# Kernel optimization log

Hardware: AMD Instinct MI355X
Metric: run time of the kernel (lower is better)

## Reference

```python
import jax, jax.numpy as jnp
import numpy as np

B, SQ, SK = 2, 2048, 2048
E = 256   # embed_dim (also per-head key dim in this MHA)
S = 256   # srcdim (also per-head value dim)
NH = 8    # num_heads
HID = 2 * S  # FFN hidden = in_dim * 2


def setup_inputs() -> dict:
    key = jax.random.key(0)
    ks = jax.random.split(key, 12)
    def w(k, shape, s=0.02):
        return jax.random.normal(k, shape, dtype=jnp.float32) * s
    return {
        "Q": jax.random.normal(ks[0], (B, SQ, E), dtype=jnp.float32),
        "H": jax.random.normal(ks[1], (B, SK, E), dtype=jnp.float32),
        "A": jax.random.normal(ks[2], (B, SK, S), dtype=jnp.float32),
        # MHA params (torch Linear convention: y = x @ W.T + b)
        "wq": w(ks[3], (NH * E, E)), "bq": jnp.zeros((NH * E,), jnp.float32),
        "wk": w(ks[4], (NH * E, E)), "bk": jnp.zeros((NH * E,), jnp.float32),
        "wv": w(ks[5], (NH * S, S)), "bv": jnp.zeros((NH * S,), jnp.float32),
        "wo": w(ks[6], (S, NH * S)), "bo": jnp.zeros((S,), jnp.float32),
        # Attension scale (Parameter(torch.ones(1)))
        "attn_scale": jnp.ones((), jnp.float32),
        # shared LayerNormA params
        "ln_g": jnp.ones((S,), jnp.float32), "ln_b": jnp.zeros((S,), jnp.float32),
        # FFN params
        "w1": w(ks[7], (HID, S)), "b1": jnp.zeros((HID,), jnp.float32),
        "w2": w(ks[8], (S, HID)), "b2": jnp.zeros((S,), jnp.float32),
    }


def _layernorm(x, g, b, eps=1e-5):
    m = x.mean(-1, keepdims=True)
    v = ((x - m) ** 2).mean(-1, keepdims=True)
    return (x - m) / jnp.sqrt(v + eps) * g + b


def reference(Q, H, A, wq, bq, wk, bk, wv, bv, wo, bo,
              attn_scale, ln_g, ln_b, w1, b1, w2, b2):
    b_, sq, _ = Q.shape
    sk = H.shape[1]
    # ---- MHA branch (A_m) ----
    q = (Q @ wq.T + bq).reshape(b_, sq, NH, E).transpose(0, 2, 1, 3)  # [b,h,sq,E]
    k = (H @ wk.T + bk).reshape(b_, sk, NH, E).transpose(0, 2, 1, 3)  # [b,h,sk,E]
    v = (A @ wv.T + bv).reshape(b_, sk, NH, S).transpose(0, 2, 1, 3)  # [b,h,sk,S]
    scores = jnp.einsum('bhqe,bhke->bhqk', q, k) / jnp.sqrt(jnp.float32(E))
    probs = jax.nn.softmax(scores, axis=-1)
    ctx = jnp.einsum('bhqk,bhkd->bhqd', probs, v)          # [b,h,sq,S]
    ctx = ctx.transpose(0, 2, 1, 3).reshape(b_, sq, NH * S)
    A_m = ctx @ wo.T + bo                                   # [b,sq,S]
    # ---- Attension branch (dot score with learned scalar scale) ----
    s2 = jnp.einsum('bqe,bke->bqk', Q, H) * attn_scale      # [b,sq,sk]
    attn_out = jax.nn.softmax(s2, axis=-1) @ A              # [b,sq,S]
    # ---- residual + LN + FFN + LN (shared LayerNormA) ----
    Ad = _layernorm(A_m + attn_out, ln_g, ln_b)
    ff = jax.nn.relu(Ad @ w1.T + b1) @ w2.T + b2
    return _layernorm(ff + Ad, ln_g, ln_b)
```

## Files before the change

### kernel.cpp

```cpp
#include <hip/hip_runtime.h>
#include <cstdint>
#include <cstddef>


typedef unsigned short u16;
typedef __attribute__((ext_vector_type(8))) short bf16x8;
typedef __attribute__((ext_vector_type(4))) short s16x4;
typedef __attribute__((ext_vector_type(4))) float f32x4;

__device__ __forceinline__ float b2f(u16 u){
  union { unsigned int i; float f; } v; v.i = ((unsigned int)u) << 16; return v.f;
}
__device__ __forceinline__ u16 f2b(float f){
  union { float f; unsigned int i; } v; v.f = f;
  unsigned int u = v.i;
  unsigned int r = (u + 0x7FFFu + ((u >> 16) & 1u)) >> 16;
  return (u16)r;
}
__device__ __forceinline__ f32x4 mfma16(bf16x8 a, bf16x8 b, f32x4 c){
  return __builtin_amdgcn_mfma_f32_16x16x32_bf16(a, b, c, 0, 0, 0);
}
__device__ __forceinline__ void gload_lds16(const void* g, void* l){
  __builtin_amdgcn_global_load_lds(
      (const __attribute__((address_space(1))) unsigned int*)g,
      (__attribute__((address_space(3))) unsigned int*)l, 16, 0, 0);
}

__global__ void detect_kernel(const u16* __restrict__ q, int* __restrict__ flag){
  __shared__ int cnt;
  if (threadIdx.x == 0) cnt = 0;
  __syncthreads();
  int c = 0;
  for (int i = threadIdx.x; i < 2048; i += 256){
    u16 u = q[i];
    int e = (u >> 7) & 0xFF;
    if (e >= 140) c++;
  }
  atomicAdd(&cnt, c);
  __syncthreads();
  if (threadIdx.x == 0) *flag = (cnt > 64) ? 1 : 0;
}

struct ConvJobs {
  const void* src[18];
  void*       dst[18];
  void*       dst2[18];
  int         n[18];
  int         mode[18];
};

__global__ void convert_all(ConvJobs J, const int* __restrict__ flag){
  const int j = blockIdx.y;
  const int n = J.n[j];
  const int mode = J.mode[j];
  const int isf = *flag;
  for (int i = blockIdx.x * blockDim.x + threadIdx.x; i < n; i += gridDim.x * blockDim.x){
    if (mode == 2){
      float f = isf ? ((const float*)J.src[j])[i] : b2f(((const u16*)J.src[j])[i]);
      ((float*)J.dst[j])[i] = f;
    } else {
      u16 hi, lo = 0;
      if (isf){
        float f = ((const float*)J.src[j])[i];
        hi = f2b(f);
        if (mode == 1) lo = f2b(f - b2f(hi));
      } else {
        hi = ((const u16*)J.src[j])[i];
      }
      ((u16*)J.dst[j])[i] = hi;
      if (mode == 1) ((u16*)J.dst2[j])[i] = lo;
    }
  }
}

template<int STORE, bool RELU>
__global__ __launch_bounds__(256) void gemm_bt(
    const u16* __restrict__ X, const u16* __restrict__ W,
    const float* __restrict__ bias, void* __restrict__ outp,
    int M, int N, int K)
{
  __shared__ __align__(16) u16 lx[128 * 64];
  __shared__ __align__(16) u16 lw[128 * 64];
  const int tid = threadIdx.x;
  const int l = tid & 63, w = tid >> 6;
  const int lg = l >> 4, lr = l & 15;
  const int wr = w >> 1, wc = w & 1;
  const int m0 = blockIdx.x * 128;
  const int n0 = blockIdx.y * 128;

  f32x4 acc[4][4];
#pragma unroll
  for (int mi = 0; mi < 4; mi++)
#pragma unroll
    for (int ni = 0; ni < 4; ni++) acc[mi][ni] = (f32x4){0.f, 0.f, 0.f, 0.f};

  const int nkt = K >> 6;
  for (int kt = 0; kt < nkt; ++kt){
    __syncthreads();
#pragma unroll
    for (int it = 0; it < 4; ++it){
      int c = it * 256 + tid;
      int row = c >> 3, j = c & 7;
      int sj = (j ^ (row & 7)) * 8;
      const u16* gx = X + (size_t)(m0 + row) * K + kt * 64 + sj;
      gload_lds16(gx, (char*)lx + c * 16);
      const u16* gw = W + (size_t)(n0 + row) * K + kt * 64 + sj;
      gload_lds16(gw, (char*)lw + c * 16);
    }
    __syncthreads();
#pragma unroll
    for (int ks = 0; ks < 2; ++ks){
      bf16x8 af[4], bfv[4];
      const int swz = ((ks * 4 + lg) ^ (lr & 7)) * 8;
#pragma unroll
      for (int mi = 0; mi < 4; mi++)
        af[mi] = *(const bf16x8*)(lx + (wr * 64 + mi * 16 + lr) * 64 + swz);
#pragma unroll
      for (int ni = 0; ni < 4; ni++)
        bfv[ni] = *(const bf16x8*)(lw + (wc * 64 + ni * 16 + lr) * 64 + swz);
#pragma unroll
      for (int mi = 0; mi < 4; mi++)
#pragma unroll
        for (int ni = 0; ni < 4; ni++)
          acc[mi][ni] = mfma16(af[mi], bfv[ni], acc[mi][ni]);
    }
  }

#pragma unroll
  for (int mi = 0; mi < 4; mi++)
#pragma unroll
    for (int ni = 0; ni < 4; ni++){
      const int gr0 = m0 + wr * 64 + mi * 16 + lg * 4;
      const int gc  = n0 + wc * 64 + ni * 16 + lr;
      const float bv = bias ? bias[gc] : 0.f;
      if (STORE == 2){
        const int b = gr0 >> 11, sk0 = gr0 & 2047;
        const int h = gc >> 8,  d   = gc & 255;
        s16x4 pk;
#pragma unroll
        for (int r = 0; r < 4; r++){
          float v = acc[mi][ni][r] + bv;
          pk[r] = (short)f2b(v);
        }
        *(s16x4*)((u16*)outp + ((size_t)((b << 3) + h) * 256 + d) * 2048 + sk0) = pk;
      } else {
#pragma unroll
        for (int r = 0; r < 4; r++){
          float v = acc[mi][ni][r] + bv;
          if (RELU) v = fmaxf(v, 0.f);
          size_t idx = (size_t)(gr0 + r) * N + gc;
          if (STORE == 0) ((u16*)outp)[idx] = f2b(v);
          else            ((float*)outp)[idx] = v;
        }
      }
    }
}

template<int STORE, bool RELU>
__global__ __launch_bounds__(256) void gemm_bt64(
    const u16* __restrict__ X, const u16* __restrict__ W,
    const float* __restrict__ bias, void* __restrict__ outp,
    int M, int N, int K)
{
  __shared__ __align__(16) u16 lx[64 * 64];
  __shared__ __align__(16) u16 lw[64 * 64];
  const int tid = threadIdx.x;
  const int l = tid & 63, w = tid >> 6;
  const int lg = l >> 4, lr = l & 15;
  const int wr = w >> 1, wc = w & 1;
  const int m0 = blockIdx.x * 64;
  const int n0 = blockIdx.y * 64;

  f32x4 acc[2][2];
#pragma unroll
  for (int mi = 0; mi < 2; mi++)
#pragma unroll
    for (int ni = 0; ni < 2; ni++) acc[mi][ni] = (f32x4){0.f, 0.f, 0.f, 0.f};

  const int nkt = K >> 6;
  for (int kt = 0; kt < nkt; ++kt){
    __syncthreads();
#pragma unroll
    for (int it = 0; it < 2; ++it){
      int c = it * 256 + tid;
      int row = c >> 3, j = c & 7;
      int sj = (j ^ (row & 7)) * 8;
      const u16* gx = X + (size_t)(m0 + row) * K + kt * 64 + sj;
      gload_lds16(gx, (char*)lx + c * 16);
      const u16* gw = W + (size_t)(n0 + row) * K + kt * 64 + sj;
      gload_lds16(gw, (char*)lw + c * 16);
    }
    __syncthreads();
#pragma unroll
    for (int ks = 0; ks < 2; ++ks){
      bf16x8 af[2], bfv[2];
      const int swz = ((ks * 4 + lg) ^ (lr & 7)) * 8;
#pragma unroll
      for (int mi = 0; mi < 2; mi++)
        af[mi] = *(const bf16x8*)(lx + (wr * 32 + mi * 16 + lr) * 64 + swz);
#pragma unroll
      for (int ni = 0; ni < 2; ni++)
        bfv[ni] = *(const bf16x8*)(lw + (wc * 32 + ni * 16 + lr) * 64 + swz);
#pragma unroll
      for (int mi = 0; mi < 2; mi++)
#pragma unroll
        for (int ni = 0; ni < 2; ni++)
          acc[mi][ni] = mfma16(af[mi], bfv[ni], acc[mi][ni]);
    }
  }

#pragma unroll
  for (int mi = 0; mi < 2; mi++)
#pragma unroll
    for (int ni = 0; ni < 2; ni++){
      const int gr0 = m0 + wr * 32 + mi * 16 + lg * 4;
      const int gc  = n0 + wc * 32 + ni * 16 + lr;
      const float bv = bias ? bias[gc] : 0.f;
#pragma unroll
      for (int r = 0; r < 4; r++){
        float v = acc[mi][ni][r] + bv;
        if (RELU) v = fmaxf(v, 0.f);
        size_t idx = (size_t)(gr0 + r) * N + gc;
        if (STORE == 0) ((u16*)outp)[idx] = f2b(v);
        else            ((float*)outp)[idx] = v;
      }
    }
}

__global__ __launch_bounds__(256) void transpose_k(const u16* __restrict__ src, u16* __restrict__ dst){
  __shared__ u16 t[64][72];
  const int b   = blockIdx.z;
  const int sk0 = blockIdx.x * 64;
  const int d0  = blockIdx.y * 64;
  const int tid = threadIdx.x;
  union U8 { bf16x8 v; u16 e[8]; };
#pragma unroll
  for (int half = 0; half < 2; ++half){
    int c = half * 256 + tid;
    int r = c >> 3, c8 = (c & 7) * 8;
    U8 u; u.v = *(const bf16x8*)(src + ((size_t)b * 2048 + sk0 + r) * 256 + d0 + c8);
#pragma unroll
    for (int i = 0; i < 8; i++) t[r][c8 + i] = u.e[i];
  }
  __syncthreads();
#pragma unroll
  for (int half = 0; half < 2; ++half){
    int c = half * 256 + tid;
    int dr = c >> 3, s8 = (c & 7) * 8;
    U8 u;
#pragma unroll
    for (int i = 0; i < 8; i++) u.e[i] = t[s8 + i][dr];
    *(bf16x8*)(dst + ((size_t)b * 256 + d0 + dr) * 2048 + sk0 + s8) = u.v;
  }
}

__global__ __launch_bounds__(512, 2) void flash_mha(
    const u16* __restrict__ Qp, const u16* __restrict__ Kp,
    const u16* __restrict__ Vt, u16* __restrict__ outp)
{
  __shared__ __align__(16) u16 bufK[64 * 256];
  __shared__ __align__(16) u16 bufV[256 * 64];
  __shared__ __align__(16) u16 ldsP[8][16 * 64];
  const int tid = threadIdx.x, l = tid & 63, w = tid >> 6;
  const int lg = l >> 4, lr = l & 15;
  const int lr7 = lr & 7;
  const int bid = blockIdx.x;
  const int xcd = bid & 7;
  const int slot = bid >> 3;
  const int by = xcd * 2 + (slot >> 4);
  const int qt = slot & 15;
  const size_t qkbase = ((size_t)(by >> 3) * 2048) * 2048 + (size_t)(by & 7) * 256;
  const size_t vbase  = (size_t)by * (256 * 2048);
  const int q0 = qt * 128 + w * 16;

  bf16x8 qf[8];
#pragma unroll
  for (int ks = 0; ks < 8; ks++)
    qf[ks] = *(const bf16x8*)(Qp + qkbase +
        (size_t)(q0 + lr) * 2048 + ks * 32 + lg * 8);

  float mrun[4], lpart[4];
#pragma unroll
  for (int r = 0; r < 4; r++){ mrun[r] = -3e38f; lpart[r] = 0.f; }
  f32x4 accO[16];
#pragma unroll
  for (int db = 0; db < 16; db++) accO[db] = (f32x4){0.f, 0.f, 0.f, 0.f};

  auto stageK = [&](int kv0){
#pragma unroll
    for (int it = 0; it < 4; ++it){
      int c = it * 512 + tid;
      int row = c >> 5, j = c & 31;
      const u16* g = Kp + qkbase + (size_t)(kv0 + row) * 2048 + (j ^ (row & 7)) * 8;
      gload_lds16(g, (char*)bufK + c * 16);
    }
  };
  auto stageV = [&](int kv0){
#pragma unroll
    for (int it = 0; it < 4; ++it){
      int c = it * 512 + tid;
      int row = c >> 3, j = c & 7;
      const u16* g = Vt + vbase + (size_t)row * 2048 + kv0 + (j ^ (row & 7)) * 8;
      gload_lds16(g, (char*)bufV + c * 16);
    }
  };

  stageK(0);

  for (int t = 0; t < 32; ++t){
    const int kv0 = t * 64;
    __syncthreads();
    stageV(kv0);

    f32x4 s[4];
#pragma unroll
    for (int kb = 0; kb < 4; kb++) s[kb] = (f32x4){0.f, 0.f, 0.f, 0.f};

    __builtin_amdgcn_s_setprio(1);
#pragma unroll
    for (int ks = 0; ks < 8; ks++){
      bf16x8 bfr[4];
      const int swz = (((ks * 4 + lg) ^ lr7)) * 8;
#pragma unroll
      for (int kb = 0; kb < 4; kb++)
        bfr[kb] = *(const bf16x8*)(bufK + (kb * 16 + lr) * 256 + swz);
#pragma unroll
      for (int kb = 0; kb < 4; kb++)
        s[kb] = mfma16(qf[ks], bfr[kb], s[kb]);
    }
    __builtin_amdgcn_s_setprio(0);

    float pm[4];
#pragma unroll
    for (int kb = 0; kb < 4; kb++)
#pragma unroll
      for (int r = 0; r < 4; r++) s[kb][r] *= 0.0625f;
#pragma unroll
    for (int r = 0; r < 4; r++)
      pm[r] = fmaxf(fmaxf(s[0][r], s[1][r]), fmaxf(s[2][r], s[3][r]));
#pragma unroll
    for (int m = 1; m < 16; m <<= 1)
#pragma unroll
      for (int r = 0; r < 4; r++) pm[r] = fmaxf(pm[r], __shfl_xor(pm[r], m));

    float gmax = fmaxf(fmaxf(pm[0] - mrun[0], pm[1] - mrun[1]),
                       fmaxf(pm[2] - mrun[2], pm[3] - mrun[3]));
    if (__any(gmax > 8.0f)){
#pragma unroll
      for (int r = 0; r < 4; r++){
        float mn = fmaxf(mrun[r], pm[r]);
        float corr = __expf(mrun[r] - mn);
        mrun[r] = mn;
        lpart[r] *= corr;
#pragma unroll
        for (int db = 0; db < 16; db++) accO[db][r] *= corr;
      }
    }
#pragma unroll
    for (int kb = 0; kb < 4; kb++)
#pragma unroll
      for (int r = 0; r < 4; r++){
        float p = __expf(s[kb][r] - mrun[r]);
        lpart[r] += p;
        const int row = lg * 4 + r;
        ldsP[w][(row << 6) + (((kb * 2 + (lr >> 3)) ^ (row & 7)) << 3) + (lr & 7)] = f2b(p);
      }

    __syncthreads();
    if (t + 1 < 32) stageK(kv0 + 64);

    __builtin_amdgcn_s_setprio(1);
#pragma unroll
    for (int ks2 = 0; ks2 < 2; ++ks2){
      bf16x8 pa = *(const bf16x8*)(ldsP[w] + (lr << 6) + (((ks2 * 4 + lg) ^ lr7) << 3));
      const int swz = (((ks2 * 4 + lg) ^ lr7)) * 8;
#pragma unroll
      for (int db = 0; db < 16; ++db){
        bf16x8 vb = *(const bf16x8*)(bufV + (db * 16 + lr) * 64 + swz);
        accO[db] = mfma16(pa, vb, accO[db]);
      }
    }
    __builtin_amdgcn_s_setprio(0);
  }

  float lrun[4];
#pragma unroll
  for (int r = 0; r < 4; r++) lrun[r] = lpart[r];
#pragma unroll
  for (int m = 1; m < 16; m <<= 1)
#pragma unroll
    for (int r = 0; r < 4; r++) lrun[r] += __shfl_xor(lrun[r], m);
  float inv[4];
#pragma unroll
  for (int r = 0; r < 4; r++) inv[r] = 1.f / lrun[r];
#pragma unroll
  for (int db = 0; db < 16; db++)
#pragma unroll
    for (int r = 0; r < 4; r++){
      float v = accO[db][r] * inv[r];
      int q = q0 + lg * 4 + r;
      int d = db * 16 + lr;
      outp[((size_t)(by >> 3) * 2048 + q) * 2048 + (size_t)(by & 7) * 256 + d] = f2b(v);
    }
}

__global__ __launch_bounds__(256) void flash_b2(
    const u16* __restrict__ Qh, const u16* __restrict__ Ql,
    const u16* __restrict__ Kh, const u16* __restrict__ Kl,
    const u16* __restrict__ Vt,
    float* __restrict__ Opart, float* __restrict__ mlp,
    const float* __restrict__ p_scale, const int* __restrict__ flagp)
{
  __shared__ __align__(16) u16 bufK[64 * 256];
  __shared__ __align__(16) u16 bufV[256 * 64];
  __shared__ __align__(16) u16 ldsP[4][16 * 72];
  const int tid = threadIdx.x, l = tid & 63, w = tid >> 6;
  const int lg = l >> 4, lr = l & 15;
  const int lr7 = lr & 7;
  const int by = blockIdx.y, qt = blockIdx.x, kc = blockIdx.z;
  const size_t qkbase = (size_t)by * (2048 * 256);
  const size_t vbase  = (size_t)by * (256 * 2048);
  const float scale = *p_scale;
  const int split = *flagp;
  const int kvbase = kc * 256;
  const int q0 = qt * 64 + w * 16;

  bf16x8 qf[8], qfl[8];
#pragma unroll
  for (int ks = 0; ks < 8; ks++)
    qf[ks] = *(const bf16x8*)(Qh + qkbase + (size_t)(q0 + lr) * 256 + ks * 32 + lg * 8);
  if (split){
#pragma unroll
    for (int ks = 0; ks < 8; ks++)
      qfl[ks] = *(const bf16x8*)(Ql + qkbase + (size_t)(q0 + lr) * 256 + ks * 32 + lg * 8);
  } else {
#pragma unroll
    for (int ks = 0; ks < 8; ks++) qfl[ks] = qf[ks];
  }

  float mrun[4], lpart[4];
#pragma unroll
  for (int r = 0; r < 4; r++){ mrun[r] = -3e38f; lpart[r] = 0.f; }
  f32x4 accO[16];
#pragma unroll
  for (int db = 0; db < 16; db++) accO[db] = (f32x4){0.f, 0.f, 0.f, 0.f};

  auto stageK = [&](const u16* __restrict__ src, int kv0){
#pragma unroll
    for (int it = 0; it < 8; ++it){
      int c = it * 256 + tid;
      int row = c >> 5, j = c & 31;
      const u16* g = src + qkbase + (size_t)(kv0 + row) * 256 + (j ^ (row & 7)) * 8;
      gload_lds16(g, (char*)bufK + c * 16);
    }
  };
  auto stageV = [&](int kv0){
#pragma unroll
    for (int it = 0; it < 8; ++it){
      int c = it * 256 + tid;
      int row = c >> 3, j = c & 7;
      const u16* g = Vt + vbase + (size_t)row * 2048 + kv0 + (j ^ (row & 7)) * 8;
      gload_lds16(g, (char*)bufV + c * 16);
    }
  };

  for (int t = 0; t < 4; ++t){
    const int kv0 = kvbase + t * 64;
    __syncthreads();
    stageK(Kh, kv0);
    stageV(kv0);
    __syncthreads();

    f32x4 s[4];
#pragma unroll
    for (int kb = 0; kb < 4; kb++) s[kb] = (f32x4){0.f, 0.f, 0.f, 0.f};
#pragma unroll
    for (int ks = 0; ks < 8; ks++){
      bf16x8 bfr[4];
      const int swz = (((ks * 4 + lg) ^ lr7)) * 8;
#pragma unroll
      for (int kb = 0; kb < 4; kb++)
        bfr[kb] = *(const bf16x8*)(bufK + (kb * 16 + lr) * 256 + swz);
#pragma unroll
      for (int kb = 0; kb < 4; kb++) s[kb] = mfma16(qf[ks], bfr[kb], s[kb]);
      if (split){
#pragma unroll
        for (int kb = 0; kb < 4; kb++) s[kb] = mfma16(qfl[ks], bfr[kb], s[kb]);
      }
    }
    if (split){
      __syncthreads();
      stageK(Kl, kv0);
      __syncthreads();
#pragma unroll
      for (int ks = 0; ks < 8; ks++){
        bf16x8 bfr[4];
        const int swz = (((ks * 4 + lg) ^ lr7)) * 8;
#pragma unroll
        for (int kb = 0; kb < 4; kb++)
          bfr[kb] = *(const bf16x8*)(bufK + (kb * 16 + lr) * 256 + swz);
#pragma unroll
        for (int kb = 0; kb < 4; kb++) s[kb] = mfma16(qf[ks], bfr[kb], s[kb]);
      }
    }

#pragma unroll
    for (int kb = 0; kb < 4; kb++)
#pragma unroll
      for (int r = 0; r < 4; r++) s[kb][r] *= scale;

    float pm[4];
#pragma unroll
    for (int r = 0; r < 4; r++)
      pm[r] = fmaxf(fmaxf(s[0][r], s[1][r]), fmaxf(s[2][r], s[3][r]));
#pragma unroll
    for (int m = 1; m < 16; m <<= 1)
#pragma unroll
      for (int r = 0; r < 4; r++) pm[r] = fmaxf(pm[r], __shfl_xor(pm[r], m));

    float g = fmaxf(fmaxf(pm[0] - mrun[0], pm[1] - mrun[1]),
                    fmaxf(pm[2] - mrun[2], pm[3] - mrun[3]));
    if (__any(g > 8.0f)){
#pragma unroll
      for (int r = 0; r < 4; r++){
        float mn = fmaxf(mrun[r], pm[r]);
        float corr = __expf(mrun[r] - mn);
        mrun[r] = mn;
        lpart[r] *= corr;
#pragma unroll
        for (int db = 0; db < 16; db++) accO[db][r] *= corr;
      }
    }
#pragma unroll
    for (int kb = 0; kb < 4; kb++)
#pragma unroll
      for (int r = 0; r < 4; r++){
        float p = __expf(s[kb][r] - mrun[r]);
        lpart[r] += p;
        ldsP[w][(lg * 4 + r) * 72 + kb * 16 + lr] = f2b(p);
      }

#pragma unroll
    for (int ks2 = 0; ks2 < 2; ++ks2){
      bf16x8 pa = *(const bf16x8*)(ldsP[w] + lr * 72 + ks2 * 32 + lg * 8);
      const int swz = (((ks2 * 4 + lg) ^ lr7)) * 8;
#pragma unroll
      for (int db = 0; db < 16; ++db){
        bf16x8 vb = *(const bf16x8*)(bufV + (db * 16 + lr) * 64 + swz);
        accO[db] = mfma16(pa, vb, accO[db]);
      }
    }
  }

  float lrun[4];
#pragma unroll
  for (int r = 0; r < 4; r++) lrun[r] = lpart[r];
#pragma unroll
  for (int m = 1; m < 16; m <<= 1)
#pragma unroll
    for (int r = 0; r < 4; r++) lrun[r] += __shfl_xor(lrun[r], m);

#pragma unroll
  for (int db = 0; db < 16; db++)
#pragma unroll
    for (int r = 0; r < 4; r++){
      int q = q0 + lg * 4 + r;
      int d = db * 16 + lr;
      Opart[((size_t)((kc * 2 + by) * 2048 + q)) * 256 + d] = accO[db][r];
    }
  if (lr == 0){
#pragma unroll
    for (int r = 0; r < 4; r++){
      int idx = (kc * 2 + by) * 2048 + q0 + lg * 4 + r;
      mlp[idx] = mrun[r];
      mlp[32768 + idx] = lrun[r];
    }
  }
}

__global__ __launch_bounds__(256) void merge_k(
    const float* __restrict__ Opart, const float* __restrict__ ml,
    float* __restrict__ outp)
{
  const int w = threadIdx.x >> 6, l = threadIdx.x & 63;
  const int row = blockIdx.x * 4 + w;
  const int b = row >> 11, q = row & 2047;
  float m[8], li[8], M = -3e38f;
#pragma unroll
  for (int kc = 0; kc < 8; kc++){
    int idx = (kc * 2 + b) * 2048 + q;
    m[kc] = ml[idx];
    li[kc] = ml[32768 + idx];
    M = fmaxf(M, m[kc]);
  }
  float L = 0.f, wgt[8];
#pragma unroll
  for (int kc = 0; kc < 8; kc++){ wgt[kc] = __expf(m[kc] - M); L += li[kc] * wgt[kc]; }
  const float invL = 1.f / L;
  f32x4 o = (f32x4){0.f, 0.f, 0.f, 0.f};
#pragma unroll
  for (int kc = 0; kc < 8; kc++){
    f32x4 v = *(const f32x4*)(Opart + ((size_t)((kc * 2 + b) * 2048 + q)) * 256 + l * 4);
#pragma unroll
    for (int i = 0; i < 4; i++) o[i] += v[i] * wgt[kc];
  }
#pragma unroll
  for (int i = 0; i < 4; i++) o[i] *= invL;
  *(f32x4*)(outp + (size_t)row * 256 + l * 4) = o;
}

template<int RESF32, int OUTFLAG>
__global__ __launch_bounds__(256) void ln_k(
    const float* __restrict__ x, const void* __restrict__ res,
    const float* __restrict__ g, const float* __restrict__ bb,
    void* __restrict__ outp, const int* __restrict__ flagp)
{
  const int w = threadIdx.x >> 6, l = threadIdx.x & 63;
  const int row = blockIdx.x * 4 + w;
  const size_t off = (size_t)row * 256 + l * 4;
  f32x4 xv = *(const f32x4*)(x + off);
  float v[4];
  if (RESF32){
    f32x4 rv = *(const f32x4*)((const float*)res + off);
#pragma unroll
    for (int i = 0; i < 4; i++) v[i] = xv[i] + rv[i];
  } else {
    const u16* rp = (const u16*)res + off;
#pragma unroll
    for (int i = 0; i < 4; i++) v[i] = xv[i] + b2f(rp[i]);
  }
  float s = 0.f, sq = 0.f;
#pragma unroll
  for (int i = 0; i < 4; i++){ s += v[i]; sq += v[i] * v[i]; }
  for (int m = 1; m < 64; m <<= 1){ s += __shfl_xor(s, m); sq += __shfl_xor(sq, m); }
  const float mean = s * (1.f / 256.f);
  const float var = sq * (1.f / 256.f) - mean * mean;
  const float rstd = rsqrtf(var + 1e-5f);
  float y[4];
#pragma unroll
  for (int i = 0; i < 4; i++) y[i] = (v[i] - mean) * rstd * g[l * 4 + i] + bb[l * 4 + i];
  const bool f32out = OUTFLAG && (*flagp);
  if (f32out){
    f32x4 o;
#pragma unroll
    for (int i = 0; i < 4; i++) o[i] = y[i];
    *(f32x4*)((float*)outp + off) = o;
  } else {
    s16x4 o;
#pragma unroll
    for (int i = 0; i < 4; i++) o[i] = (short)f2b(y[i]);
    *(s16x4*)((u16*)outp + off) = o;
  }
}

extern "C" void kernel_launch(void* const* d_in, const int* in_sizes, int n_in,
                              void* d_out, int out_size, void* d_ws, size_t ws_size,
                              hipStream_t stream)
{
  (void)in_sizes; (void)n_in; (void)out_size; (void)ws_size;
  char* ws = (char*)d_ws;
  size_t off = 0;
  auto alloc = [&](size_t bytes) -> char* {
    char* p = ws + off;
    off += (bytes + 255) & ~(size_t)255;
    return p;
  };
  int*   flag    = (int*)  alloc(4);
  float* p_scale = (float*)alloc(4);
  float* p_bq    = (float*)alloc(2048 * 4);
  float* p_bk    = (float*)alloc(2048 * 4);
  float* p_bv    = (float*)alloc(2048 * 4);
  float* p_bo    = (float*)alloc(256 * 4);
  float* p_b1    = (float*)alloc(512 * 4);
  float* p_b2    = (float*)alloc(256 * 4);
  float* p_g     = (float*)alloc(256 * 4);
  float* p_b     = (float*)alloc(256 * 4);
  u16* Qc  = (u16*)alloc((size_t)1048576 * 2);
  u16* Qlo = (u16*)alloc((size_t)1048576 * 2);
  u16* Hc  = (u16*)alloc((size_t)1048576 * 2);
  u16* Hlo = (u16*)alloc((size_t)1048576 * 2);
  u16* Ac  = (u16*)alloc((size_t)1048576 * 2);
  u16* wqc = (u16*)alloc((size_t)524288 * 2);
  u16* wkc = (u16*)alloc((size_t)524288 * 2);
  u16* wvc = (u16*)alloc((size_t)524288 * 2);
  u16* woc = (u16*)alloc((size_t)524288 * 2);
  u16* w1c = (u16*)alloc((size_t)131072 * 2);
  u16* w2c = (u16*)alloc((size_t)131072 * 2);
  u16* qbuf = (u16*)alloc((size_t)4096 * 2048 * 2);
  u16* kbuf = (u16*)alloc((size_t)4096 * 2048 * 2);
  u16* vtb  = (u16*)alloc((size_t)4096 * 2048 * 2);
  u16* ctx  = (u16*)alloc((size_t)4096 * 2048 * 2);
  u16* At   = (u16*)alloc((size_t)1048576 * 2);
  float* attn_o = (float*)alloc((size_t)4096 * 256 * 4);
  float* Am     = (float*)alloc((size_t)4096 * 256 * 4);
  u16* Ad  = (u16*)alloc((size_t)1048576 * 2);
  u16* h1  = (u16*)alloc((size_t)4096 * 512 * 2);
  float* ffb = (float*)alloc((size_t)4096 * 256 * 4);

  detect_kernel<<<1, 256, 0, stream>>>((const u16*)d_in[0], flag);

  ConvJobs J{};
  auto setj = [&](int i, const void* s, void* d, void* d2, int n, int m){
    J.src[i] = s; J.dst[i] = d; J.dst2[i] = d2; J.n[i] = n; J.mode[i] = m;
  };
  setj(0,  d_in[0],  Qc,  Qlo, 1048576, 1);
  setj(1,  d_in[1],  Hc,  Hlo, 1048576, 1);
  setj(2,  d_in[2],  Ac,  nullptr, 1048576, 0);
  setj(3,  d_in[3],  wqc, nullptr, 524288, 0);
  setj(4,  d_in[5],  wkc, nullptr, 524288, 0);
  setj(5,  d_in[7],  wvc, nullptr, 524288, 0);
  setj(6,  d_in[9],  woc, nullptr, 524288, 0);
  setj(7,  d_in[14], w1c, nullptr, 131072, 0);
  setj(8,  d_in[16], w2c, nullptr, 131072, 0);
  setj(9,  d_in[4],  p_bq, nullptr, 2048, 2);
  setj(10, d_in[6],  p_bk, nullptr, 2048, 2);
  setj(11, d_in[8],  p_bv, nullptr, 2048, 2);
  setj(12, d_in[10], p_bo, nullptr, 256, 2);
  setj(13, d_in[15], p_b1, nullptr, 512, 2);
  setj(14, d_in[17], p_b2, nullptr, 256, 2);
  setj(15, d_in[12], p_g,  nullptr, 256, 2);
  setj(16, d_in[13], p_b,  nullptr, 256, 2);
  setj(17, d_in[11], p_scale, nullptr, 1, 2);
  convert_all<<<dim3(64, 18), 256, 0, stream>>>(J, flag);

  gemm_bt<0, false><<<dim3(32, 16), 256, 0, stream>>>(Qc, wqc, p_bq, qbuf, 4096, 2048, 256);
  gemm_bt<0, false><<<dim3(32, 16), 256, 0, stream>>>(Hc, wkc, p_bk, kbuf, 4096, 2048, 256);
  gemm_bt<2, false><<<dim3(32, 16), 256, 0, stream>>>(Ac, wvc, p_bv, vtb,  4096, 2048, 256);
  transpose_k<<<dim3(32, 4, 2), 256, 0, stream>>>(Ac, At);

  flash_mha<<<dim3(256), 512, 0, stream>>>(qbuf, kbuf, vtb, ctx);

  float* Opart = (float*)qbuf;
  float* mlbuf = (float*)vtb;
  flash_b2<<<dim3(32, 2, 8), 256, 0, stream>>>(Qc, Qlo, Hc, Hlo, At,
                                               Opart, mlbuf, p_scale, flag);
  merge_k<<<1024, 256, 0, stream>>>(Opart, mlbuf, attn_o);

  gemm_bt64<1, false><<<dim3(64, 4), 256, 0, stream>>>(ctx, woc, p_bo, Am, 4096, 256, 2048);
  ln_k<1, 0><<<1024, 256, 0, stream>>>(Am, attn_o, p_g, p_b, Ad, flag);
  gemm_bt64<0, true ><<<dim3(64, 8), 256, 0, stream>>>(Ad, w1c, p_b1, h1, 4096, 512, 256);
  gemm_bt64<1, false><<<dim3(64, 4), 256, 0, stream>>>(h1, w2c, p_b2, ffb, 4096, 256, 512);
  ln_k<0, 1><<<1024, 256, 0, stream>>>(ffb, Ad, p_g, p_b, d_out, flag);
}
```

Measured before the change: 289.5 us.

## Double-buffer K and V tiles in flash MHA with prefetch two steps ahead

```diff
diff --git a/kernel.cpp b/kernel.cpp
--- a/kernel.cpp
+++ b/kernel.cpp
@@ -258,8 +258,8 @@
     const u16* __restrict__ Qp, const u16* __restrict__ Kp,
     const u16* __restrict__ Vt, u16* __restrict__ outp)
 {
-  __shared__ __align__(16) u16 bufK[64 * 256];
-  __shared__ __align__(16) u16 bufV[256 * 64];
+  __shared__ __align__(16) u16 bufK[2][64 * 256];
+  __shared__ __align__(16) u16 bufV[2][256 * 64];
   __shared__ __align__(16) u16 ldsP[8][16 * 64];
   const int tid = threadIdx.x, l = tid & 63, w = tid >> 6;
   const int lg = l >> 4, lr = l & 15;
@@ -286,31 +286,34 @@
 #pragma unroll
   for (int db = 0; db < 16; db++) accO[db] = (f32x4){0.f, 0.f, 0.f, 0.f};
 
-  auto stageK = [&](int kv0){
+  auto stageK = [&](int kv0, u16* dst){
 #pragma unroll
     for (int it = 0; it < 4; ++it){
       int c = it * 512 + tid;
       int row = c >> 5, j = c & 31;
       const u16* g = Kp + qkbase + (size_t)(kv0 + row) * 2048 + (j ^ (row & 7)) * 8;
-      gload_lds16(g, (char*)bufK + c * 16);
+      gload_lds16(g, (char*)dst + c * 16);
     }
   };
-  auto stageV = [&](int kv0){
+  auto stageV = [&](int kv0, u16* dst){
 #pragma unroll
     for (int it = 0; it < 4; ++it){
       int c = it * 512 + tid;
       int row = c >> 3, j = c & 7;
       const u16* g = Vt + vbase + (size_t)row * 2048 + kv0 + (j ^ (row & 7)) * 8;
-      gload_lds16(g, (char*)bufV + c * 16);
+      gload_lds16(g, (char*)dst + c * 16);
     }
   };
 
-  stageK(0);
+  stageK(0,  bufK[0]); stageV(0,  bufV[0]);
+  stageK(64, bufK[1]); stageV(64, bufV[1]);
 
   for (int t = 0; t < 32; ++t){
     const int kv0 = t * 64;
-    __syncthreads();
-    stageV(kv0);
+    const int cur = t & 1;
+    if (t < 31) asm volatile("s_waitcnt vmcnt(8)" ::: "memory");
+    else        asm volatile("s_waitcnt vmcnt(0)" ::: "memory");
+    asm volatile("s_barrier" ::: "memory");
 
     f32x4 s[4];
 #pragma unroll
@@ -323,7 +326,7 @@
       const int swz = (((ks * 4 + lg) ^ lr7)) * 8;
 #pragma unroll
       for (int kb = 0; kb < 4; kb++)
-        bfr[kb] = *(const bf16x8*)(bufK + (kb * 16 + lr) * 256 + swz);
+        bfr[kb] = *(const bf16x8*)(bufK[cur] + (kb * 16 + lr) * 256 + swz);
 #pragma unroll
       for (int kb = 0; kb < 4; kb++)
         s[kb] = mfma16(qf[ks], bfr[kb], s[kb]);
@@ -366,9 +369,6 @@
         ldsP[w][(row << 6) + (((kb * 2 + (lr >> 3)) ^ (row & 7)) << 3) + (lr & 7)] = f2b(p);
       }
 
-    __syncthreads();
-    if (t + 1 < 32) stageK(kv0 + 64);
-
     __builtin_amdgcn_s_setprio(1);
 #pragma unroll
     for (int ks2 = 0; ks2 < 2; ++ks2){
@@ -376,11 +376,17 @@
       const int swz = (((ks2 * 4 + lg) ^ lr7)) * 8;
 #pragma unroll
       for (int db = 0; db < 16; ++db){
-        bf16x8 vb = *(const bf16x8*)(bufV + (db * 16 + lr) * 64 + swz);
+        bf16x8 vb = *(const bf16x8*)(bufV[cur] + (db * 16 + lr) * 64 + swz);
         accO[db] = mfma16(pa, vb, accO[db]);
       }
     }
     __builtin_amdgcn_s_setprio(0);
+
+    asm volatile("s_barrier" ::: "memory");
+    if (t + 2 < 32){
+      stageK(kv0 + 128, bufK[cur]);
+      stageV(kv0 + 128, bufV[cur]);
+    }
   }
 
   float lrun[4];
```

New measurement: 287.6 us. About the same (-0.7%).
